# Kernel tuning notes

Measured on AMD Instinct MI355X. Metric: run time of the kernel, lower is better.

Reference implementation:

```python
import jax, jax.numpy as jnp
import numpy as np

N, H, E, A, T = 50000, 128, 800000, 16, 4


def setup_inputs() -> dict:
    key = jax.random.key(0)
    ks = jax.random.split(key, 12)
    s = 1.0 / np.sqrt(H + A)
    s2 = 1.0 / np.sqrt(H)
    return {
        "h": jax.random.normal(ks[0], (N, H), dtype=jnp.float32),
        "edge_index": jax.random.randint(ks[1], (2, E), 0, N, dtype=jnp.int32),
        "edge_type": jax.random.randint(ks[2], (E,), 0, T, dtype=jnp.int32),
        "edge_attr": jax.random.normal(ks[3], (E, A), dtype=jnp.float32),
        # per-edge-type 2-layer MLP params
        "W1": jax.random.uniform(ks[4], (T, H + A, H), minval=-s, maxval=s, dtype=jnp.float32),
        "b1": jax.random.uniform(ks[5], (T, H), minval=-s, maxval=s, dtype=jnp.float32),
        "W2": jax.random.uniform(ks[6], (T, H, H), minval=-s2, maxval=s2, dtype=jnp.float32),
        "b2": jax.random.uniform(ks[7], (T, H), minval=-s2, maxval=s2, dtype=jnp.float32),
        # GRUCell params (torch layout: [3H, H] with gate order r, z, n)
        "w_ih": jax.random.uniform(ks[8], (3 * H, H), minval=-s2, maxval=s2, dtype=jnp.float32),
        "w_hh": jax.random.uniform(ks[9], (3 * H, H), minval=-s2, maxval=s2, dtype=jnp.float32),
        "b_ih": jax.random.uniform(ks[10], (3 * H,), minval=-s2, maxval=s2, dtype=jnp.float32),
        "b_hh": jax.random.uniform(ks[11], (3 * H,), minval=-s2, maxval=s2, dtype=jnp.float32),
    }


def reference(h, edge_index, edge_type, edge_attr, W1, b1, W2, b2, w_ih, w_hh, b_ih, b_hh):
    src, dst = edge_index[0], edge_index[1]
    h_in = jnp.concatenate([h[src], edge_attr], axis=-1)  # [E, H+A]
    # per-edge-type MLP; loop over small fixed num_edge_types, mask-select
    m = jnp.zeros((h_in.shape[0], H), dtype=h.dtype)
    for t in range(T):
        mt = jax.nn.relu(h_in @ W1[t] + b1[t]) @ W2[t] + b2[t]  # [E, H]
        m = jnp.where((edge_type == t)[:, None], mt, m)
    # scatter-add messages to destination nodes
    msg = jax.ops.segment_sum(m, dst, num_segments=h.shape[0])  # [N, H]
    # GRUCell(msg, h) with torch gate order r, z, n
    gi = msg @ w_ih.T + b_ih  # [N, 3H]
    gh = h @ w_hh.T + b_hh
    i_r, i_z, i_n = jnp.split(gi, 3, axis=-1)
    h_r, h_z, h_n = jnp.split(gh, 3, axis=-1)
    r = jax.nn.sigmoid(i_r + h_r)
    z = jax.nn.sigmoid(i_z + h_z)
    n = jnp.tanh(i_n + r * h_n)
    return (1.0 - z) * n + z * h
```

## Files before the change

kernel.cpp:

```cpp
#include <hip/hip_runtime.h>
#include <stdint.h>

#define Hh 128
#define Aa 16
#define Tt 4
#define K1 144
#define K1P 160
#define W1T_LD 168
#define WG_LD  136

typedef float f32x4 __attribute__((ext_vector_type(4)));
typedef __bf16 bf16x8 __attribute__((ext_vector_type(8)));
typedef unsigned short u16x8 __attribute__((ext_vector_type(8)));
typedef unsigned short u16x4 __attribute__((ext_vector_type(4)));
typedef unsigned short u16x2 __attribute__((ext_vector_type(2)));

static __device__ __forceinline__ unsigned short f2bf(float f) {
    unsigned u = __builtin_bit_cast(unsigned, f);
    u += 0x7fffu + ((u >> 16) & 1u);
    return (unsigned short)(u >> 16);
}

static __device__ __forceinline__ float bf2f(unsigned short u) {
    return __builtin_bit_cast(float, (unsigned)u << 16);
}

static __device__ __forceinline__ bf16x8 pack8(const float* __restrict__ x) {
    f32x4 a = *(const f32x4*)x;
    f32x4 b = *(const f32x4*)(x + 4);
    u16x8 t;
    t[0] = f2bf(a[0]); t[1] = f2bf(a[1]); t[2] = f2bf(a[2]); t[3] = f2bf(a[3]);
    t[4] = f2bf(b[0]); t[5] = f2bf(b[1]); t[6] = f2bf(b[2]); t[7] = f2bf(b[3]);
    return __builtin_bit_cast(bf16x8, t);
}

static __device__ __forceinline__ bf16x8 zero_bf8() {
    u16x8 z = {0, 0, 0, 0, 0, 0, 0, 0};
    return __builtin_bit_cast(bf16x8, z);
}

__global__ void cast_all_kernel(
    const float* __restrict__ h, const float* __restrict__ W2,
    const float* __restrict__ wih, const float* __restrict__ whh,
    unsigned short* __restrict__ h_bf, unsigned short* __restrict__ W2bf,
    unsigned short* __restrict__ wihb, unsigned short* __restrict__ whhb,
    int n0, int n1, int n2, int n3)
{
    int i = blockIdx.x * blockDim.x + threadIdx.x;
    if (i >= n3) return;
    const float* s; unsigned short* d; int off;
    if (i < n0)      { s = h;   d = h_bf; off = i; }
    else if (i < n1) { s = W2;  d = W2bf; off = i - n0; }
    else if (i < n2) { s = wih; d = wihb; off = i - n1; }
    else             { s = whh; d = whhb; off = i - n2; }
    f32x4 v = *(const f32x4*)(s + (size_t)off * 4);
    u16x4 o;
    o[0] = f2bf(v[0]); o[1] = f2bf(v[1]); o[2] = f2bf(v[2]); o[3] = f2bf(v[3]);
    *(u16x4*)(d + (size_t)off * 4) = o;
}

__global__ void w1t_kernel(const float* __restrict__ W1, unsigned short* __restrict__ W1Tbf) {
    __shared__ float tile[16][129];
    const int b = blockIdx.x;
    const int t = b / 10, kb = b % 10;
    const int k0 = kb * 16;
    const int tid = threadIdx.x;
    for (int e = tid; e < 16 * 128; e += 256) {
        int k = e >> 7, n = e & 127;
        tile[k][n] = (k0 + k < K1) ? W1[((size_t)t * K1 + k0 + k) * Hh + n] : 0.f;
    }
    __syncthreads();
    for (int e = tid; e < 128 * 16; e += 256) {
        int n = e >> 4, kk = e & 15;
        W1Tbf[((size_t)t * Hh + n) * K1P + k0 + kk] = f2bf(tile[kk][n]);
    }
}

__global__ void hist_kernel(const int* __restrict__ et, const int* __restrict__ eidx,
                            int E, int N, int* __restrict__ cnt, unsigned* __restrict__ rank) {
    for (int i = blockIdx.x * blockDim.x + threadIdx.x; i < E; i += gridDim.x * blockDim.x) {
        int tt = et[i];
        unsigned rD = (unsigned)atomicAdd(&cnt[tt * N + eidx[E + i]], 1);
        unsigned rS = (unsigned)atomicAdd(&cnt[4 * N + tt * N + eidx[i]], 1);
        rank[i] = rD | (rS << 16);
    }
}

__global__ void scanA_kernel(const int* __restrict__ deg2, int nb, int* __restrict__ bsum) {
    __shared__ int red[256];
    const int t = threadIdx.x;
    const int i0 = blockIdx.x * 1024 + t * 4;
    int s = 0;
    #pragma unroll
    for (int j = 0; j < 4; j++) if (i0 + j < nb) s += deg2[i0 + j];
    red[t] = s; __syncthreads();
    for (int d = 128; d > 0; d >>= 1) {
        if (t < d) red[t] += red[t + d];
        __syncthreads();
    }
    if (t == 0) bsum[blockIdx.x] = red[0];
}

__global__ void scanB_kernel(int* __restrict__ bsum, int nblocks,
                             int* __restrict__ rowptrD, int fourN, int E) {
    __shared__ int ts[512];
    const int t = threadIdx.x;
    int v = (t < nblocks) ? bsum[t] : 0;
    ts[t] = v; __syncthreads();
    for (int d = 1; d < 512; d <<= 1) {
        int x = (t >= d) ? ts[t - d] : 0;
        __syncthreads();
        ts[t] += x;
        __syncthreads();
    }
    if (t < nblocks) bsum[t] = ts[t] - v;
    if (t == 0) rowptrD[fourN] = E;
}

__global__ void scanC_kernel(int* __restrict__ cur, int nb, int fourN,
                             const int* __restrict__ bsum, int* __restrict__ rowptrD) {
    __shared__ int ts[256];
    const int t = threadIdx.x;
    const int i0 = blockIdx.x * 1024 + t * 4;
    int v[4];
    #pragma unroll
    for (int j = 0; j < 4; j++) v[j] = (i0 + j < nb) ? cur[i0 + j] : 0;
    int s = v[0] + v[1] + v[2] + v[3];
    ts[t] = s; __syncthreads();
    for (int d = 1; d < 256; d <<= 1) {
        int x = (t >= d) ? ts[t - d] : 0;
        __syncthreads();
        ts[t] += x;
        __syncthreads();
    }
    int run = bsum[blockIdx.x] + ts[t] - s;
    #pragma unroll
    for (int j = 0; j < 4; j++) {
        if (i0 + j < nb) {
            if (i0 + j < fourN) rowptrD[i0 + j] = run;
            cur[i0 + j] = run;
            run += v[j];
        }
    }
}

__global__ void fill2_kernel(const int* __restrict__ et, const int* __restrict__ eidx,
                             int E, int N, const int* __restrict__ binstart,
                             const unsigned* __restrict__ rank, int4* __restrict__ rec) {
    for (int i = blockIdx.x * blockDim.x + threadIdx.x; i < E; i += gridDim.x * blockDim.x) {
        int tt = et[i];
        int d = eidx[E + i], s = eidx[i];
        unsigned r = rank[i];
        int posD = binstart[tt * N + d] + (int)(r & 0xffffu);
        int posS = binstart[4 * N + tt * N + s] + (int)(r >> 16) - E;
        rec[posS] = make_int4(s, i, posD, 0);
    }
}

__global__ __launch_bounds__(512) void l1_kernel(
    const unsigned short* __restrict__ h_bf, const int4* __restrict__ rec,
    const float* __restrict__ eattr, const unsigned short* __restrict__ W1Tbf,
    const float* __restrict__ b1, const int* __restrict__ rowptrD,
    unsigned short* __restrict__ Yg, int N)
{
    __shared__ unsigned short W1T[128 * W1T_LD];
    __shared__ float b1s[128];
    const int t = blockIdx.x & 3;
    const int lb = blockIdx.x >> 2;
    const int nbk = gridDim.x >> 2;
    const int tid = threadIdx.x;

    for (int idx = tid; idx < (Hh * K1P) / 8; idx += 512) {
        int n = idx / (K1P / 8), c = (idx % (K1P / 8)) * 8;
        *(u16x8*)&W1T[n * W1T_LD + c] =
            *(const u16x8*)&W1Tbf[((size_t)t * Hh + n) * K1P + c];
    }
    if (tid < 128) b1s[tid] = b1[t * Hh + tid];
    __syncthreads();

    const int tstart = rowptrD[t * N];
    const int tend = rowptrD[(t + 1) * N];
    const int cnt = tend - tstart;
    const int ntiles = (cnt + 127) >> 7;
    const int lane = tid & 63;
    const int eg = tid >> 7;
    const int mh = (tid >> 6) & 1;
    const int l15 = lane & 15, q = lane >> 4;
    const int mtb = mh * 4;

    for (int tile = lb; tile < ntiles; tile += nbk) {
        const int p0 = tstart + tile * 128 + eg * 32;
        const int pa = p0 + l15, pb = p0 + 16 + l15;
        const bool va = pa < tend, vb = pb < tend;
        const int4 ra = rec[va ? pa : tstart];
        const int4 rb = rec[vb ? pb : tstart];
        const unsigned short* __restrict__ hA = h_bf + (size_t)ra.x * Hh;
        const unsigned short* __restrict__ hB = h_bf + (size_t)rb.x * Hh;

        f32x4 acc[4][2];
        #pragma unroll
        for (int mt = 0; mt < 4; mt++) {
            acc[mt][0] = (f32x4){0.f, 0.f, 0.f, 0.f};
            acc[mt][1] = (f32x4){0.f, 0.f, 0.f, 0.f};
        }

        #pragma unroll
        for (int ks = 0; ks < 5; ks++) {
            const int k0 = ks * 32;
            bf16x8 fb_a, fb_b;
            if (ks < 4) {
                fb_a = __builtin_bit_cast(bf16x8, *(const u16x8*)(hA + k0 + q * 8));
                fb_b = __builtin_bit_cast(bf16x8, *(const u16x8*)(hB + k0 + q * 8));
            } else if (q < 2) {
                fb_a = pack8(eattr + (size_t)ra.y * Aa + q * 8);
                fb_b = pack8(eattr + (size_t)rb.y * Aa + q * 8);
            } else {
                fb_a = zero_bf8();
                fb_b = zero_bf8();
            }
            #pragma unroll
            for (int mt = 0; mt < 4; mt++) {
                bf16x8 fa = *(const bf16x8*)&W1T[((mtb + mt) * 16 + l15) * W1T_LD + k0 + q * 8];
                acc[mt][0] = __builtin_amdgcn_mfma_f32_16x16x32_bf16(fa, fb_a, acc[mt][0], 0, 0, 0);
                acc[mt][1] = __builtin_amdgcn_mfma_f32_16x16x32_bf16(fa, fb_b, acc[mt][1], 0, 0, 0);
            }
        }

        #pragma unroll
        for (int g = 0; g < 2; g++) {
            if (g ? vb : va) {
                const int yp = g ? rb.z : ra.z;
                unsigned short* __restrict__ o = Yg + (size_t)yp * Hh + mtb * 16 + q * 4;
                #pragma unroll
                for (int mt = 0; mt < 4; mt++) {
                    f32x4 bias = *(const f32x4*)&b1s[(mtb + mt) * 16 + q * 4];
                    u16x4 y;
                    #pragma unroll
                    for (int i = 0; i < 4; i++) {
                        float v = acc[mt][g][i] + bias[i];
                        y[i] = f2bf(v > 0.f ? v : 0.f);
                    }
                    *(u16x4*)(o + mt * 16) = y;
                }
            }
        }
    }
}

__global__ __launch_bounds__(256) void zgemm_kernel(
    const unsigned short* __restrict__ Yg, const int* __restrict__ rowptrD,
    const unsigned short* __restrict__ W2bf, const float* __restrict__ b2,
    unsigned short* __restrict__ msgb, int N)
{
    __shared__ unsigned short W2T[128 * WG_LD];
    __shared__ float b2s[512];
    __shared__ int cntS[4 * 64];
    const int tid = threadIdx.x;
    const int w = tid >> 6, lane = tid & 63;
    const int l15 = lane & 15, q = lane >> 4;
    const int nodebase = blockIdx.x * 64 + w * 16;
    const int nA = min(nodebase + l15, N - 1);

    if (tid < 512) {
        b2s[tid] = b2[tid];
        b2s[tid + 256] = b2[tid + 256];
    }

    f32x4 acc[8];
    #pragma unroll
    for (int ct = 0; ct < 8; ct++) acc[ct] = (f32x4){0.f, 0.f, 0.f, 0.f};

    for (int t = 0; t < Tt; t++) {
        __syncthreads();
        for (int idx = tid; idx < Hh * Hh; idx += 256) {
            int k = idx >> 7, n = idx & 127;
            W2T[n * WG_LD + k] = W2bf[((size_t)t * Hh + k) * Hh + n];
        }
        __syncthreads();

        const int seg = rowptrD[(size_t)t * N + nA];
        const int len = rowptrD[(size_t)t * N + nA + 1] - seg;
        cntS[w * 64 + t * 16 + l15] = len;

        float asum[32];
        #pragma unroll
        for (int i = 0; i < 32; i++) asum[i] = 0.f;
        for (int j = 0; j < len; j++) {
            const unsigned short* __restrict__ yr = Yg + (size_t)(seg + j) * Hh;
            #pragma unroll
            for (int ks = 0; ks < 4; ks++) {
                u16x8 yv = *(const u16x8*)(yr + ks * 32 + q * 8);
                #pragma unroll
                for (int e = 0; e < 8; e++) asum[ks * 8 + e] += bf2f(yv[e]);
            }
        }

        #pragma unroll
        for (int ks = 0; ks < 4; ks++) {
            u16x8 fr;
            #pragma unroll
            for (int e = 0; e < 8; e++) fr[e] = f2bf(asum[ks * 8 + e]);
            bf16x8 fa = __builtin_bit_cast(bf16x8, fr);
            #pragma unroll
            for (int ct = 0; ct < 8; ct++) {
                bf16x8 fb = *(const bf16x8*)&W2T[(ct * 16 + l15) * WG_LD + ks * 32 + q * 8];
                acc[ct] = __builtin_amdgcn_mfma_f32_16x16x32_bf16(fa, fb, acc[ct], 0, 0, 0);
            }
        }
    }
    __syncthreads();

    #pragma unroll
    for (int ct = 0; ct < 8; ct++) {
        const int c = ct * 16 + l15;
        #pragma unroll
        for (int i = 0; i < 4; i++) {
            int node = nodebase + q * 4 + i;
            if (node < N) {
                float bias = 0.f;
                #pragma unroll
                for (int t = 0; t < Tt; t++)
                    bias += (float)cntS[w * 64 + t * 16 + q * 4 + i] * b2s[t * 128 + c];
                msgb[(size_t)node * Hh + c] = f2bf(acc[ct][i] + bias);
            }
        }
    }
}

__global__ __launch_bounds__(512) void gru_kernel(
    const float* __restrict__ h, const unsigned short* __restrict__ h_bf,
    const unsigned short* __restrict__ msgb,
    const unsigned short* __restrict__ wihb, const unsigned short* __restrict__ whhb,
    const float* __restrict__ b_ih, const float* __restrict__ b_hh,
    float* __restrict__ out, int N)
{
    __shared__ unsigned short Wg[128 * WG_LD];
    const int tid = threadIdx.x;
    const int w = tid >> 6, lane = tid & 63;
    const int l15 = lane & 15, q = lane >> 4;
    const int nodebase = blockIdx.x * 128 + w * 16;
    const int nA = min(nodebase + l15, N - 1);

    bf16x8 fm[4], fh[4];
    #pragma unroll
    for (int ks = 0; ks < 4; ks++) {
        fm[ks] = __builtin_bit_cast(bf16x8, *(const u16x8*)(msgb + (size_t)nA * Hh + ks * 32 + q * 8));
        fh[ks] = __builtin_bit_cast(bf16x8, *(const u16x8*)(h_bf + (size_t)nA * Hh + ks * 32 + q * 8));
    }

    f32x4 gr[8], gz[8], gin[8], ghn[8];
    #pragma unroll
    for (int ct = 0; ct < 8; ct++) {
        gr[ct] = (f32x4){0.f, 0.f, 0.f, 0.f};
        gz[ct] = (f32x4){0.f, 0.f, 0.f, 0.f};
        gin[ct] = (f32x4){0.f, 0.f, 0.f, 0.f};
        ghn[ct] = (f32x4){0.f, 0.f, 0.f, 0.f};
    }

    auto stage = [&](const unsigned short* __restrict__ Ws, int gate) {
        __syncthreads();
        for (int idx = tid; idx < (Hh * Hh) / 8; idx += 512) {
            int o = idx >> 4, k8 = (idx & 15) * 8;
            *(u16x8*)&Wg[o * WG_LD + k8] =
                *(const u16x8*)&Ws[(size_t)gate * Hh * Hh + o * Hh + k8];
        }
        __syncthreads();
    };
    auto matmul = [&](f32x4* acc, const bf16x8* fa) {
        #pragma unroll
        for (int ks = 0; ks < 4; ks++) {
            #pragma unroll
            for (int ct = 0; ct < 8; ct++) {
                bf16x8 fb = *(const bf16x8*)&Wg[(ct * 16 + l15) * WG_LD + ks * 32 + q * 8];
                acc[ct] = __builtin_amdgcn_mfma_f32_16x16x32_bf16(fa[ks], fb, acc[ct], 0, 0, 0);
            }
        }
    };

    stage(wihb, 0); matmul(gr, fm);
    stage(whhb, 0); matmul(gr, fh);
    stage(wihb, 1); matmul(gz, fm);
    stage(whhb, 1); matmul(gz, fh);
    stage(wihb, 2); matmul(gin, fm);
    stage(whhb, 2); matmul(ghn, fh);

    #pragma unroll
    for (int ct = 0; ct < 8; ct++) {
        int c = ct * 16 + l15;
        float bir = b_ih[c],       bhr = b_hh[c];
        float biz = b_ih[128 + c], bhz = b_hh[128 + c];
        float bin = b_ih[256 + c], bhn = b_hh[256 + c];
        #pragma unroll
        for (int i = 0; i < 4; i++) {
            int node = nodebase + q * 4 + i;
            if (node < N) {
                float rv = 1.f / (1.f + __expf(-(gr[ct][i] + bir + bhr)));
                float zv = 1.f / (1.f + __expf(-(gz[ct][i] + biz + bhz)));
                float npre = gin[ct][i] + bin + rv * (ghn[ct][i] + bhn);
                float e2 = __expf(-2.f * npre);
                float nv = (1.f - e2) / (1.f + e2);
                float hv = h[(size_t)node * Hh + c];
                out[(size_t)node * Hh + c] = (1.f - zv) * nv + zv * hv;
            }
        }
    }
}

static inline size_t align256(size_t x) { return (x + 255) & ~(size_t)255; }

extern "C" void kernel_launch(void* const* d_in, const int* in_sizes, int n_in,
                              void* d_out, int out_size, void* d_ws, size_t ws_size,
                              hipStream_t stream)
{
    const float* h     = (const float*)d_in[0];
    const int*   eidx  = (const int*)d_in[1];
    const int*   et    = (const int*)d_in[2];
    const float* eattr = (const float*)d_in[3];
    const float* W1    = (const float*)d_in[4];
    const float* b1    = (const float*)d_in[5];
    const float* W2    = (const float*)d_in[6];
    const float* b2    = (const float*)d_in[7];
    const float* w_ih  = (const float*)d_in[8];
    const float* w_hh  = (const float*)d_in[9];
    const float* b_ih  = (const float*)d_in[10];
    const float* b_hh  = (const float*)d_in[11];

    const int N = in_sizes[0] / Hh;
    const int E = in_sizes[1] / 2;
    const int nb = 8 * N;
    const int sblocks = (nb + 1023) / 1024;

    char* p = (char*)d_ws;
    unsigned short* msgb = (unsigned short*)p; p += align256((size_t)N * Hh * sizeof(unsigned short));
    unsigned short* Yg = (unsigned short*)p;   p += align256((size_t)E * Hh * sizeof(unsigned short));
    int4* rec = (int4*)p;               p += align256((size_t)E * sizeof(int4));
    unsigned* rank = (unsigned*)p;      p += align256((size_t)E * sizeof(unsigned));
    int* rowptrD = (int*)p;             p += align256(((size_t)4 * N + 1) * sizeof(int));
    int* cur = (int*)p;                 p += align256((size_t)nb * sizeof(int));
    int* bsum = (int*)p;                p += align256(1024 * sizeof(int));
    unsigned short* h_bf = (unsigned short*)p; p += align256((size_t)N * Hh * sizeof(unsigned short));
    unsigned short* W1Tbf = (unsigned short*)p; p += align256((size_t)Tt * Hh * K1P * sizeof(unsigned short));
    unsigned short* W2bf = (unsigned short*)p; p += align256((size_t)Tt * Hh * Hh * sizeof(unsigned short));
    unsigned short* wihb = (unsigned short*)p; p += align256((size_t)3 * Hh * Hh * sizeof(unsigned short));
    unsigned short* whhb = (unsigned short*)p; p += align256((size_t)3 * Hh * Hh * sizeof(unsigned short));

    hipMemsetAsync(cur, 0, (size_t)nb * sizeof(int), stream);

    {
        int n4h = N * Hh / 4, n42 = Tt * Hh * Hh / 4, n4g = 3 * Hh * Hh / 4;
        int c0 = n4h, c1 = c0 + n42, c2 = c1 + n4g, c3 = c2 + n4g;
        cast_all_kernel<<<(c3 + 255) / 256, 256, 0, stream>>>(
            h, W2, w_ih, w_hh, h_bf, W2bf, wihb, whhb, c0, c1, c2, c3);
    }
    w1t_kernel<<<Tt * 10, 256, 0, stream>>>(W1, W1Tbf);

    hist_kernel<<<1024, 256, 0, stream>>>(et, eidx, E, N, cur, rank);
    scanA_kernel<<<sblocks, 256, 0, stream>>>(cur, nb, bsum);
    scanB_kernel<<<1, 512, 0, stream>>>(bsum, sblocks, rowptrD, 4 * N, E);
    scanC_kernel<<<sblocks, 256, 0, stream>>>(cur, nb, 4 * N, bsum, rowptrD);
    fill2_kernel<<<1024, 256, 0, stream>>>(et, eidx, E, N, cur, rank, rec);

    l1_kernel<<<2048, 512, 0, stream>>>(h_bf, rec, eattr, W1Tbf, b1, rowptrD, Yg, N);
    zgemm_kernel<<<(N + 63) / 64, 256, 0, stream>>>(Yg, rowptrD, W2bf, b2, msgb, N);

    int gblocks = (N + 127) / 128;
    gru_kernel<<<gblocks, 512, 0, stream>>>(h, h_bf, msgb, wihb, whhb, b_ih, b_hh, (float*)d_out, N);
}
```

Baseline: 502.4 us.

## Split segment-sum into its own kernel, pre-transpose W2, retile L1 and pipeline GRU weight staging

Several changes land together. W2 is now transposed and cast once by a dedicated kernel, so the second GEMM stages weights with vector copies. The per-segment reduction of layer-1 outputs moves out of the GEMM into a separate sumY kernel that writes the sum over the first row, and the GEMM then reads only that row. The layer-1 kernel is retiled so each wave covers all 128 output columns for 32 edges, with 256-edge tiles, half the grid, and a minimum of 4 waves per SIMD requested in launch bounds. The GRU kernel prefetches the next gate's weights into registers while the current matmul runs, and finalises the r/n gates early to free accumulator registers. The extra kernel launch and the in-place write into Yg add overhead, and the sumY loop may be imbalanced across threads.

```diff
diff --git a/kernel.cpp b/kernel.cpp
--- a/kernel.cpp
+++ b/kernel.cpp
@@ -40,19 +40,16 @@
 }
 
 __global__ void cast_all_kernel(
-    const float* __restrict__ h, const float* __restrict__ W2,
-    const float* __restrict__ wih, const float* __restrict__ whh,
-    unsigned short* __restrict__ h_bf, unsigned short* __restrict__ W2bf,
-    unsigned short* __restrict__ wihb, unsigned short* __restrict__ whhb,
-    int n0, int n1, int n2, int n3)
+    const float* __restrict__ h, const float* __restrict__ wih, const float* __restrict__ whh,
+    unsigned short* __restrict__ h_bf, unsigned short* __restrict__ wihb,
+    unsigned short* __restrict__ whhb, int n0, int n1, int n2)
 {
     int i = blockIdx.x * blockDim.x + threadIdx.x;
-    if (i >= n3) return;
+    if (i >= n2) return;
     const float* s; unsigned short* d; int off;
     if (i < n0)      { s = h;   d = h_bf; off = i; }
-    else if (i < n1) { s = W2;  d = W2bf; off = i - n0; }
-    else if (i < n2) { s = wih; d = wihb; off = i - n1; }
-    else             { s = whh; d = whhb; off = i - n2; }
+    else if (i < n1) { s = wih; d = wihb; off = i - n0; }
+    else             { s = whh; d = whhb; off = i - n1; }
     f32x4 v = *(const f32x4*)(s + (size_t)off * 4);
     u16x4 o;
     o[0] = f2bf(v[0]); o[1] = f2bf(v[1]); o[2] = f2bf(v[2]); o[3] = f2bf(v[3]);
@@ -73,6 +70,23 @@
     for (int e = tid; e < 128 * 16; e += 256) {
         int n = e >> 4, kk = e & 15;
         W1Tbf[((size_t)t * Hh + n) * K1P + k0 + kk] = f2bf(tile[kk][n]);
+    }
+}
+
+__global__ void w2t_kernel(const float* __restrict__ W2, unsigned short* __restrict__ W2Tbf) {
+    __shared__ float tile[16][129];
+    const int b = blockIdx.x;
+    const int t = b >> 3, kb = b & 7;
+    const int k0 = kb * 16;
+    const int tid = threadIdx.x;
+    for (int e = tid; e < 16 * 128; e += 256) {
+        int k = e >> 7, n = e & 127;
+        tile[k][n] = W2[((size_t)t * Hh + k0 + k) * Hh + n];
+    }
+    __syncthreads();
+    for (int e = tid; e < 128 * 16; e += 256) {
+        int n = e >> 4, kk = e & 15;
+        W2Tbf[((size_t)t * Hh + n) * Hh + k0 + kk] = f2bf(tile[kk][n]);
     }
 }
 
@@ -157,7 +171,7 @@
     }
 }
 
-__global__ __launch_bounds__(512) void l1_kernel(
+__global__ __launch_bounds__(512, 4) void l1_kernel(
     const unsigned short* __restrict__ h_bf, const int4* __restrict__ rec,
     const float* __restrict__ eattr, const unsigned short* __restrict__ W1Tbf,
     const float* __restrict__ b1, const int* __restrict__ rowptrD,
@@ -171,7 +185,7 @@
     const int tid = threadIdx.x;
 
     for (int idx = tid; idx < (Hh * K1P) / 8; idx += 512) {
-        int n = idx / (K1P / 8), c = (idx % (K1P / 8)) * 8;
+        int n = idx / 20, c = (idx % 20) * 8;
         *(u16x8*)&W1T[n * W1T_LD + c] =
             *(const u16x8*)&W1Tbf[((size_t)t * Hh + n) * K1P + c];
     }
@@ -181,25 +195,22 @@
     const int tstart = rowptrD[t * N];
     const int tend = rowptrD[(t + 1) * N];
     const int cnt = tend - tstart;
-    const int ntiles = (cnt + 127) >> 7;
-    const int lane = tid & 63;
-    const int eg = tid >> 7;
-    const int mh = (tid >> 6) & 1;
+    const int ntiles = (cnt + 255) >> 8;
+    const int w = tid >> 6, lane = tid & 63;
     const int l15 = lane & 15, q = lane >> 4;
-    const int mtb = mh * 4;
+    const int tl = tend - 1;
 
     for (int tile = lb; tile < ntiles; tile += nbk) {
-        const int p0 = tstart + tile * 128 + eg * 32;
-        const int pa = p0 + l15, pb = p0 + 16 + l15;
-        const bool va = pa < tend, vb = pb < tend;
-        const int4 ra = rec[va ? pa : tstart];
-        const int4 rb = rec[vb ? pb : tstart];
+        const int p0 = tstart + tile * 256 + w * 32;
+        const bool va = p0 + l15 < tend, vb = p0 + 16 + l15 < tend;
+        const int4 ra = rec[min(p0 + l15, tl)];
+        const int4 rb = rec[min(p0 + 16 + l15, tl)];
         const unsigned short* __restrict__ hA = h_bf + (size_t)ra.x * Hh;
         const unsigned short* __restrict__ hB = h_bf + (size_t)rb.x * Hh;
 
-        f32x4 acc[4][2];
-        #pragma unroll
-        for (int mt = 0; mt < 4; mt++) {
+        f32x4 acc[8][2];
+        #pragma unroll
+        for (int mt = 0; mt < 8; mt++) {
             acc[mt][0] = (f32x4){0.f, 0.f, 0.f, 0.f};
             acc[mt][1] = (f32x4){0.f, 0.f, 0.f, 0.f};
         }
@@ -219,8 +230,8 @@
                 fb_b = zero_bf8();
             }
             #pragma unroll
-            for (int mt = 0; mt < 4; mt++) {
-                bf16x8 fa = *(const bf16x8*)&W1T[((mtb + mt) * 16 + l15) * W1T_LD + k0 + q * 8];
+            for (int mt = 0; mt < 8; mt++) {
+                bf16x8 fa = *(const bf16x8*)&W1T[(mt * 16 + l15) * W1T_LD + k0 + q * 8];
                 acc[mt][0] = __builtin_amdgcn_mfma_f32_16x16x32_bf16(fa, fb_a, acc[mt][0], 0, 0, 0);
                 acc[mt][1] = __builtin_amdgcn_mfma_f32_16x16x32_bf16(fa, fb_b, acc[mt][1], 0, 0, 0);
             }
@@ -230,10 +241,10 @@
         for (int g = 0; g < 2; g++) {
             if (g ? vb : va) {
                 const int yp = g ? rb.z : ra.z;
-                unsigned short* __restrict__ o = Yg + (size_t)yp * Hh + mtb * 16 + q * 4;
+                unsigned short* __restrict__ o = Yg + (size_t)yp * Hh + q * 4;
                 #pragma unroll
-                for (int mt = 0; mt < 4; mt++) {
-                    f32x4 bias = *(const f32x4*)&b1s[(mtb + mt) * 16 + q * 4];
+                for (int mt = 0; mt < 8; mt++) {
+                    f32x4 bias = *(const f32x4*)&b1s[mt * 16 + q * 4];
                     u16x4 y;
                     #pragma unroll
                     for (int i = 0; i < 4; i++) {
@@ -247,9 +258,44 @@
     }
 }
 
-__global__ __launch_bounds__(256) void zgemm_kernel(
+__global__ __launch_bounds__(256) void sumY_kernel(
+    unsigned short* __restrict__ Yg, const int* __restrict__ rowptrD, int fourN)
+{
+    const int gid = blockIdx.x * blockDim.x + threadIdx.x;
+    const int stride = gridDim.x * blockDim.x;
+    const int total = fourN * 4;
+    for (int task = gid; task < total; task += stride) {
+        const int p = task >> 2;
+        const int q = task & 3;
+        const int seg = rowptrD[p];
+        const int len = rowptrD[p + 1] - seg;
+        if (len <= 1) continue;
+        float asum[32];
+        #pragma unroll
+        for (int i = 0; i < 32; i++) asum[i] = 0.f;
+        for (int j = 0; j < len; j++) {
+            const unsigned short* __restrict__ yr = Yg + (size_t)(seg + j) * Hh;
+            #pragma unroll
+            for (int ks = 0; ks < 4; ks++) {
+                u16x8 yv = *(const u16x8*)(yr + ks * 32 + q * 8);
+                #pragma unroll
+                for (int e = 0; e < 8; e++) asum[ks * 8 + e] += bf2f(yv[e]);
+            }
+        }
+        unsigned short* __restrict__ wr = Yg + (size_t)seg * Hh;
+        #pragma unroll
+        for (int ks = 0; ks < 4; ks++) {
+            u16x8 o;
+            #pragma unroll
+            for (int e = 0; e < 8; e++) o[e] = f2bf(asum[ks * 8 + e]);
+            *(u16x8*)(wr + ks * 32 + q * 8) = o;
+        }
+    }
+}
+
+__global__ __launch_bounds__(256) void gemm2_kernel(
     const unsigned short* __restrict__ Yg, const int* __restrict__ rowptrD,
-    const unsigned short* __restrict__ W2bf, const float* __restrict__ b2,
+    const unsigned short* __restrict__ W2Tbf, const float* __restrict__ b2,
     unsigned short* __restrict__ msgb, int N)
 {
     __shared__ unsigned short W2T[128 * WG_LD];
@@ -261,10 +307,8 @@
     const int nodebase = blockIdx.x * 64 + w * 16;
     const int nA = min(nodebase + l15, N - 1);
 
-    if (tid < 512) {
-        b2s[tid] = b2[tid];
-        b2s[tid + 256] = b2[tid + 256];
-    }
+    b2s[tid] = b2[tid];
+    b2s[tid + 256] = b2[tid + 256];
 
     f32x4 acc[8];
     #pragma unroll
@@ -272,9 +316,10 @@
 
     for (int t = 0; t < Tt; t++) {
         __syncthreads();
-        for (int idx = tid; idx < Hh * Hh; idx += 256) {
-            int k = idx >> 7, n = idx & 127;
-            W2T[n * WG_LD + k] = W2bf[((size_t)t * Hh + k) * Hh + n];
+        for (int idx = tid; idx < (Hh * Hh) / 8; idx += 256) {
+            int n = idx >> 4, c = (idx & 15) * 8;
+            *(u16x8*)&W2T[n * WG_LD + c] =
+                *(const u16x8*)&W2Tbf[((size_t)t * Hh + n) * Hh + c];
         }
         __syncthreads();
 
@@ -282,29 +327,23 @@
         const int len = rowptrD[(size_t)t * N + nA + 1] - seg;
         cntS[w * 64 + t * 16 + l15] = len;
 
-        float asum[32];
-        #pragma unroll
-        for (int i = 0; i < 32; i++) asum[i] = 0.f;
-        for (int j = 0; j < len; j++) {
-            const unsigned short* __restrict__ yr = Yg + (size_t)(seg + j) * Hh;
-            #pragma unroll
-            for (int ks = 0; ks < 4; ks++) {
-                u16x8 yv = *(const u16x8*)(yr + ks * 32 + q * 8);
-                #pragma unroll
-                for (int e = 0; e < 8; e++) asum[ks * 8 + e] += bf2f(yv[e]);
-            }
+        bf16x8 fa[4];
+        if (len > 0) {
+            const unsigned short* __restrict__ yr = Yg + (size_t)seg * Hh;
+            #pragma unroll
+            for (int ks = 0; ks < 4; ks++)
+                fa[ks] = __builtin_bit_cast(bf16x8, *(const u16x8*)(yr + ks * 32 + q * 8));
+        } else {
+            #pragma unroll
+            for (int ks = 0; ks < 4; ks++) fa[ks] = zero_bf8();
         }
 
         #pragma unroll
         for (int ks = 0; ks < 4; ks++) {
-            u16x8 fr;
-            #pragma unroll
-            for (int e = 0; e < 8; e++) fr[e] = f2bf(asum[ks * 8 + e]);
-            bf16x8 fa = __builtin_bit_cast(bf16x8, fr);
             #pragma unroll
             for (int ct = 0; ct < 8; ct++) {
                 bf16x8 fb = *(const bf16x8*)&W2T[(ct * 16 + l15) * WG_LD + ks * 32 + q * 8];
-                acc[ct] = __builtin_amdgcn_mfma_f32_16x16x32_bf16(fa, fb, acc[ct], 0, 0, 0);
+                acc[ct] = __builtin_amdgcn_mfma_f32_16x16x32_bf16(fa[ks], fb, acc[ct], 0, 0, 0);
             }
         }
     }
@@ -336,8 +375,9 @@
 {
     __shared__ unsigned short Wg[128 * WG_LD];
     const int tid = threadIdx.x;
-    const int w = tid >> 6, lane = tid & 63;
+    const int lane = tid & 63;
     const int l15 = lane & 15, q = lane >> 4;
+    const int w = tid >> 6;
     const int nodebase = blockIdx.x * 128 + w * 16;
     const int nA = min(nodebase + l15, N - 1);
 
@@ -348,22 +388,18 @@
         fh[ks] = __builtin_bit_cast(bf16x8, *(const u16x8*)(h_bf + (size_t)nA * Hh + ks * 32 + q * 8));
     }
 
-    f32x4 gr[8], gz[8], gin[8], ghn[8];
-    #pragma unroll
-    for (int ct = 0; ct < 8; ct++) {
-        gr[ct] = (f32x4){0.f, 0.f, 0.f, 0.f};
-        gz[ct] = (f32x4){0.f, 0.f, 0.f, 0.f};
-        gin[ct] = (f32x4){0.f, 0.f, 0.f, 0.f};
-        ghn[ct] = (f32x4){0.f, 0.f, 0.f, 0.f};
-    }
-
-    auto stage = [&](const unsigned short* __restrict__ Ws, int gate) {
-        __syncthreads();
-        for (int idx = tid; idx < (Hh * Hh) / 8; idx += 512) {
-            int o = idx >> 4, k8 = (idx & 15) * 8;
-            *(u16x8*)&Wg[o * WG_LD + k8] =
-                *(const u16x8*)&Ws[(size_t)gate * Hh * Hh + o * Hh + k8];
-        }
+    u16x8 pre[4];
+    const int so = tid >> 4, sk = (tid & 15) * 8;
+    auto loadg = [&](const unsigned short* __restrict__ Ws, int gate) {
+        #pragma unroll
+        for (int i = 0; i < 4; i++)
+            pre[i] = *(const u16x8*)&Ws[(size_t)gate * Hh * Hh + (size_t)(so + i * 32) * Hh + sk];
+    };
+    auto commit = [&]() {
+        __syncthreads();
+        #pragma unroll
+        for (int i = 0; i < 4; i++)
+            *(u16x8*)&Wg[(so + i * 32) * WG_LD + sk] = pre[i];
         __syncthreads();
     };
     auto matmul = [&](f32x4* acc, const bf16x8* fa) {
@@ -377,27 +413,47 @@
         }
     };
 
-    stage(wihb, 0); matmul(gr, fm);
-    stage(whhb, 0); matmul(gr, fh);
-    stage(wihb, 1); matmul(gz, fm);
-    stage(whhb, 1); matmul(gz, fh);
-    stage(wihb, 2); matmul(gin, fm);
-    stage(whhb, 2); matmul(ghn, fh);
-
+    f32x4 gr[8], gin[8], ghn[8];
     #pragma unroll
     for (int ct = 0; ct < 8; ct++) {
-        int c = ct * 16 + l15;
-        float bir = b_ih[c],       bhr = b_hh[c];
+        gr[ct] = (f32x4){0.f, 0.f, 0.f, 0.f};
+        gin[ct] = (f32x4){0.f, 0.f, 0.f, 0.f};
+        ghn[ct] = (f32x4){0.f, 0.f, 0.f, 0.f};
+    }
+
+    loadg(wihb, 0);
+    commit(); loadg(whhb, 0); matmul(gr, fm);
+    commit(); loadg(wihb, 2); matmul(gr, fh);
+    commit(); loadg(whhb, 2); matmul(gin, fm);
+    commit(); loadg(wihb, 1); matmul(ghn, fh);
+
+    #pragma unroll
+    for (int ct = 0; ct < 8; ct++) {
+        const int c = ct * 16 + l15;
+        float bir = b_ih[c], bhr = b_hh[c];
+        float bin = b_ih[256 + c], bhn = b_hh[256 + c];
+        #pragma unroll
+        for (int i = 0; i < 4; i++) {
+            float rv = 1.f / (1.f + __expf(-(gr[ct][i] + bir + bhr)));
+            gin[ct][i] = gin[ct][i] + bin + rv * (ghn[ct][i] + bhn);
+        }
+    }
+    #pragma unroll
+    for (int ct = 0; ct < 8; ct++) gr[ct] = (f32x4){0.f, 0.f, 0.f, 0.f};
+
+    commit(); loadg(whhb, 1); matmul(gr, fm);
+    commit();                 matmul(gr, fh);
+
+    #pragma unroll
+    for (int ct = 0; ct < 8; ct++) {
+        const int c = ct * 16 + l15;
         float biz = b_ih[128 + c], bhz = b_hh[128 + c];
-        float bin = b_ih[256 + c], bhn = b_hh[256 + c];
         #pragma unroll
         for (int i = 0; i < 4; i++) {
             int node = nodebase + q * 4 + i;
             if (node < N) {
-                float rv = 1.f / (1.f + __expf(-(gr[ct][i] + bir + bhr)));
-                float zv = 1.f / (1.f + __expf(-(gz[ct][i] + biz + bhz)));
-                float npre = gin[ct][i] + bin + rv * (ghn[ct][i] + bhn);
-                float e2 = __expf(-2.f * npre);
+                float zv = 1.f / (1.f + __expf(-(gr[ct][i] + biz + bhz)));
+                float e2 = __expf(-2.f * gin[ct][i]);
                 float nv = (1.f - e2) / (1.f + e2);
                 float hv = h[(size_t)node * Hh + c];
                 out[(size_t)node * Hh + c] = (1.f - zv) * nv + zv * hv;
@@ -440,19 +496,20 @@
     int* bsum = (int*)p;                p += align256(1024 * sizeof(int));
     unsigned short* h_bf = (unsigned short*)p; p += align256((size_t)N * Hh * sizeof(unsigned short));
     unsigned short* W1Tbf = (unsigned short*)p; p += align256((size_t)Tt * Hh * K1P * sizeof(unsigned short));
-    unsigned short* W2bf = (unsigned short*)p; p += align256((size_t)Tt * Hh * Hh * sizeof(unsigned short));
+    unsigned short* W2Tbf = (unsigned short*)p; p += align256((size_t)Tt * Hh * Hh * sizeof(unsigned short));
     unsigned short* wihb = (unsigned short*)p; p += align256((size_t)3 * Hh * Hh * sizeof(unsigned short));
     unsigned short* whhb = (unsigned short*)p; p += align256((size_t)3 * Hh * Hh * sizeof(unsigned short));
 
     hipMemsetAsync(cur, 0, (size_t)nb * sizeof(int), stream);
 
     {
-        int n4h = N * Hh / 4, n42 = Tt * Hh * Hh / 4, n4g = 3 * Hh * Hh / 4;
-        int c0 = n4h, c1 = c0 + n42, c2 = c1 + n4g, c3 = c2 + n4g;
-        cast_all_kernel<<<(c3 + 255) / 256, 256, 0, stream>>>(
-            h, W2, w_ih, w_hh, h_bf, W2bf, wihb, whhb, c0, c1, c2, c3);
+        int n4h = N * Hh / 4, n4g = 3 * Hh * Hh / 4;
+        int c0 = n4h, c1 = c0 + n4g, c2 = c1 + n4g;
+        cast_all_kernel<<<(c2 + 255) / 256, 256, 0, stream>>>(
+            h, w_ih, w_hh, h_bf, wihb, whhb, c0, c1, c2);
     }
     w1t_kernel<<<Tt * 10, 256, 0, stream>>>(W1, W1Tbf);
+    w2t_kernel<<<Tt * 8, 256, 0, stream>>>(W2, W2Tbf);
 
     hist_kernel<<<1024, 256, 0, stream>>>(et, eidx, E, N, cur, rank);
     scanA_kernel<<<sblocks, 256, 0, stream>>>(cur, nb, bsum);
@@ -460,8 +517,9 @@
     scanC_kernel<<<sblocks, 256, 0, stream>>>(cur, nb, 4 * N, bsum, rowptrD);
     fill2_kernel<<<1024, 256, 0, stream>>>(et, eidx, E, N, cur, rank, rec);
 
-    l1_kernel<<<2048, 512, 0, stream>>>(h_bf, rec, eattr, W1Tbf, b1, rowptrD, Yg, N);
-    zgemm_kernel<<<(N + 63) / 64, 256, 0, stream>>>(Yg, rowptrD, W2bf, b2, msgb, N);
+    l1_kernel<<<1024, 512, 0, stream>>>(h_bf, rec, eattr, W1Tbf, b1, rowptrD, Yg, N);
+    sumY_kernel<<<2048, 256, 0, stream>>>(Yg, rowptrD, 4 * N);
+    gemm2_kernel<<<(N + 63) / 64, 256, 0, stream>>>(Yg, rowptrD, W2Tbf, b2, msgb, N);
 
     int gblocks = (N + 127) / 128;
     gru_kernel<<<gblocks, 512, 0, stream>>>(h, h_bf, msgb, wihb, whhb, b_ih, b_hh, (float*)d_out, N);
```

Result: slower. 697.2 us (+38.8%).
